# Kernel optimization log

Hardware: AMD Instinct MI355X
Metric: run time of the kernel (lower is better)

## Reference

```python
import jax, jax.numpy as jnp
import numpy as np

N = 8192          # total nodes (bipartite: first half left, second half right)
E = 65536         # raw edges
D = 256           # emb_dim
H = 8             # heads
HD = D // H       # head_dim = 32
EAD = 2           # edge_attr_dim


def _init(k, shape, fan_in):
    return (jax.random.normal(k, shape, jnp.float32) / np.sqrt(fan_in)).astype(jnp.float32)


def setup_inputs() -> dict:
    key = jax.random.key(0)
    ks = jax.random.split(key, 16)
    x = jax.random.normal(ks[0], (N, D), jnp.float32)
    src = jax.random.randint(ks[1], (E,), 0, N // 2, jnp.int32)
    dst = jax.random.randint(ks[2], (E,), N // 2, N, jnp.int32)
    edge_index = jnp.stack([src, dst])                       # [2, E]
    edge_attr = jax.random.uniform(ks[3], (E, EAD), jnp.float32)
    query_mask = jax.random.randint(ks[4], (E,), 0, 2, jnp.int32).astype(bool)
    return {
        "x": x,
        "edge_index": edge_index,
        "edge_attr": edge_attr,
        "query_mask": query_mask,
        "start_right": N // 2,
        "W_kqv": _init(ks[5], (D, 3 * D), D), "b_kqv": jnp.zeros((3 * D,), jnp.float32),
        "W_edge": _init(ks[6], (EAD, D), EAD), "b_edge": jnp.zeros((D,), jnp.float32),
        "W_att1": _init(ks[7], (3 * HD, HD), 3 * HD), "b_att1": jnp.zeros((HD,), jnp.float32),
        "W_att2": _init(ks[8], (HD, 1), HD), "b_att2": jnp.zeros((1,), jnp.float32),
        "W_out": _init(ks[9], (D, D), D), "b_out": jnp.zeros((D,), jnp.float32),
        "bn_gamma": jnp.ones((D,), jnp.float32), "bn_beta": jnp.zeros((D,), jnp.float32),
    }


def _build_graph(edge_index, query_mask, n):
    """Replicates MetaGNN.forward edge preprocessing (static, int-only)."""
    ei = np.asarray(edge_index)
    qm = np.asarray(query_mask).astype(bool)
    sup = np.where(~qm)[0]                                   # support edges
    # cat([edge_index[:, support], edge_index.flip(0)], dim=1)
    src = np.concatenate([ei[0, sup], ei[1]])
    dst = np.concatenate([ei[1, sup], ei[0]])
    attr_idx = np.concatenate([sup, np.arange(ei.shape[1])])
    # remove_self_loops
    keep = src != dst
    src, dst, attr_idx = src[keep], dst[keep], attr_idx[keep]
    # add_self_loops with fill_value [0, 0]
    loops = np.arange(n)
    src = np.concatenate([src, loops])
    dst = np.concatenate([dst, loops])
    return jnp.asarray(src), jnp.asarray(dst), jnp.asarray(attr_idx)


def _layer(x, src, dst, ea, W_kqv, b_kqv, W_edge, b_edge, W_att1, b_att1,
           W_att2, b_att2, W_out, b_out, bn_gamma, bn_beta):
    n = x.shape[0]
    kqv = x @ W_kqv + b_kqv                                  # [N, 3D]
    q = kqv[dst, :D].reshape(-1, H, HD)                      # x_i (target)
    k = kqv[src, D:2 * D].reshape(-1, H, HD) / np.sqrt(HD)   # x_j (source)
    v = kqv[src, 2 * D:].reshape(-1, H, HD)
    ef = jax.nn.relu((ea @ W_edge + b_edge).reshape(-1, H, HD))
    feat = jnp.concatenate([k, q, ef], axis=-1)              # [E, H, 3*HD]
    hdn = jax.nn.relu(jnp.einsum('ehf,fd->ehd', feat, W_att1) + b_att1)
    logits = (jnp.einsum('ehd,do->eho', hdn, W_att2) + b_att2)[..., 0]  # [E, H]
    # scatter-softmax over destination node segments
    m = jax.ops.segment_max(logits, dst, num_segments=n)
    a = jnp.exp(logits - m[dst])
    s = jax.ops.segment_sum(a, dst, num_segments=n)
    alpha = a / (s[dst] + 1e-16)                             # [E, H]
    msg = (alpha[..., None] * v).reshape(-1, D) @ W_out + b_out
    out = jax.ops.segment_sum(msg, dst, num_segments=n) + x  # aggr='add' + residual
    # BatchNorm1d (training-mode batch statistics, eps=1e-5)
    mu = out.mean(axis=0)
    var = out.var(axis=0)
    return (out - mu) / jnp.sqrt(var + 1e-5) * bn_gamma + bn_beta


def reference(x, edge_index, edge_attr, query_mask, start_right,
              W_kqv, b_kqv, W_edge, b_edge, W_att1, b_att1, W_att2, b_att2,
              W_out, b_out, bn_gamma, bn_beta):
    n = x.shape[0]
    src, dst, attr_idx = _build_graph(edge_index, query_mask, n)
    ea = jnp.concatenate(
        [edge_attr[attr_idx], jnp.zeros((n, edge_attr.shape[1]), edge_attr.dtype)], axis=0)
    return _layer(x, src, dst, ea, W_kqv, b_kqv, W_edge, b_edge,
                  W_att1, b_att1, W_att2, b_att2, W_out, b_out, bn_gamma, bn_beta)
```

## Files before the change

kernel.cpp:

```cpp
#include <hip/hip_runtime.h>

#define N_NODES 8192
#define E_RAW   65536
#define NSLOT   (2*E_RAW + N_NODES)
#define DEGCAP  48
#define L_ITER  4
#define MAIN_BLKS (E_RAW / (16 * L_ITER))
#define TAIL_BLKS (N_NODES / (16 * L_ITER))

typedef __attribute__((ext_vector_type(8)))  short bf16x8;
typedef __attribute__((ext_vector_type(4)))  short bf16x4;
typedef __attribute__((ext_vector_type(4)))  float f32x4;
typedef __attribute__((ext_vector_type(16))) float f32x16;
typedef unsigned short u16;

__device__ __forceinline__ u16 f2b(float f) {
  unsigned u = __float_as_uint(f);
  u = (u + 0x7FFFu + ((u >> 16) & 1u)) >> 16;
  return (u16)u;
}
__device__ __forceinline__ float b2f(u16 b) {
  return __uint_as_float(((unsigned)b) << 16);
}

__global__ __launch_bounds__(256) void setup_k(
    const float* __restrict__ x, u16* __restrict__ xb,
    const float* __restrict__ W_kqv, const float* __restrict__ b_kqv,
    const float* __restrict__ W_att1, const float* __restrict__ b_att1,
    const float* __restrict__ W_edge, const float* __restrict__ b_edge,
    const float* __restrict__ W_out,
    u16* __restrict__ BcatT, float* __restrict__ biascat,
    u16* __restrict__ wa1t, u16* __restrict__ WoutT, float* __restrict__ beW,
    int4* __restrict__ zbase)
{
  __shared__ float tile[64][65];
  const float inv_sqrt_hd = 0.17677669529663687f;
  int bx = blockIdx.x, t = threadIdx.x;

  if (bx < 2048) {
    int i = bx * 256 + t;
    float4 v = ((const float4*)x)[i];
    ushort4 o;
    o.x = f2b(v.x); o.y = f2b(v.y); o.z = f2b(v.z); o.w = f2b(v.w);
    ((ushort4*)xb)[i] = o;
    return;
  }
  if (bx < 2836) {
    int c = bx - 2048;
    int i = t;
    if (c < 768) {
      float v;
      if (c < 256) {
        int h = c >> 5, d2 = c & 31;
        float s = 0.f;
        #pragma unroll
        for (int j = 0; j < 32; ++j)
          s += W_kqv[i*768 + 256 + h*32 + j] * W_att1[j*32 + d2];
        v = s * inv_sqrt_hd;
      } else if (c < 512) {
        int c2 = c - 256; int h = c2 >> 5, d2 = c2 & 31;
        float s = 0.f;
        #pragma unroll
        for (int j = 0; j < 32; ++j)
          s += W_kqv[i*768 + h*32 + j] * W_att1[(32+j)*32 + d2];
        v = s;
      } else {
        v = W_kqv[i*768 + c];
      }
      BcatT[(size_t)c * 256 + i] = f2b(v);
      if (i == 0) {
        float bv;
        if (c < 256) {
          int h = c >> 5, d2 = c & 31;
          float s = 0.f;
          for (int j = 0; j < 32; ++j)
            s += b_kqv[256 + h*32 + j] * W_att1[j*32 + d2];
          bv = s * inv_sqrt_hd;
        } else if (c < 512) {
          int c2 = c - 256; int h = c2 >> 5, d2 = c2 & 31;
          float s = 0.f;
          for (int j = 0; j < 32; ++j)
            s += b_kqv[h*32 + j] * W_att1[(32+j)*32 + d2];
          bv = s + b_att1[c2 & 31];
        } else {
          bv = b_kqv[c];
        }
        biascat[c] = bv;
      }
    } else if (c < 772) {
      int idx = (c - 768) * 256 + i;
      int d2 = idx >> 5, j = idx & 31;
      wa1t[idx] = f2b(W_att1[(64 + j) * 32 + d2]);
    } else {
      int b = c - 772;
      int r0 = (b >> 2) * 64, c0 = (b & 3) * 64;
      for (int idx = i; idx < 4096; idx += 256) {
        int r = idx >> 6, cc = idx & 63;
        tile[r][cc] = W_out[(size_t)(r0 + r) * 256 + c0 + cc];
      }
      __syncthreads();
      for (int idx = i; idx < 4096; idx += 256) {
        int cc = idx >> 6, r = idx & 63;
        WoutT[(size_t)(c0 + cc) * 256 + r0 + r] = f2b(tile[r][cc]);
      }
    }
    return;
  }
  if (bx == 2836) {
    int h = t >> 5, d2 = t & 31;
    float s = 0.f;
    #pragma unroll
    for (int f = 0; f < 32; ++f)
      s += fmaxf(b_edge[h*32 + f], 0.f) * W_att1[(64 + f)*32 + d2];
    beW[h*32 + d2] = s;
    return;
  }
  int i = (bx - 2837) * 256 + t;
  if (i < 2176) zbase[i] = make_int4(0, 0, 0, 0);
}

__global__ __launch_bounds__(256) void gemm_scatter_k(
    const u16* __restrict__ xb, const u16* __restrict__ BcatT,
    const float* __restrict__ biascat, u16* __restrict__ nodeF,
    const int* __restrict__ ei, const int* __restrict__ qm,
    int* __restrict__ cnt, int* __restrict__ csr)
{
  int bx = blockIdx.x, t = threadIdx.x;
  if (bx < 768) {
    int lane = t & 63, wid = t >> 6;
    int cb = bx % 12, rb = bx / 12;
    int r0 = rb * 128 + wid * 32;
    int c0 = cb * 64;
    int lr = lane & 15, lk = (lane >> 4) * 8;
    f32x4 acc0[4] = {}, acc1[4] = {};
    for (int k0 = 0; k0 < 256; k0 += 32) {
      bf16x8 a0 = *(const bf16x8*)&xb[(size_t)(r0 + lr) * 256 + k0 + lk];
      bf16x8 a1 = *(const bf16x8*)&xb[(size_t)(r0 + 16 + lr) * 256 + k0 + lk];
      bf16x8 b0 = *(const bf16x8*)&BcatT[(size_t)(c0 + lr) * 256 + k0 + lk];
      bf16x8 b1 = *(const bf16x8*)&BcatT[(size_t)(c0 + 16 + lr) * 256 + k0 + lk];
      bf16x8 b2 = *(const bf16x8*)&BcatT[(size_t)(c0 + 32 + lr) * 256 + k0 + lk];
      bf16x8 b3 = *(const bf16x8*)&BcatT[(size_t)(c0 + 48 + lr) * 256 + k0 + lk];
      acc0[0] = __builtin_amdgcn_mfma_f32_16x16x32_bf16(a0, b0, acc0[0], 0, 0, 0);
      acc0[1] = __builtin_amdgcn_mfma_f32_16x16x32_bf16(a0, b1, acc0[1], 0, 0, 0);
      acc0[2] = __builtin_amdgcn_mfma_f32_16x16x32_bf16(a0, b2, acc0[2], 0, 0, 0);
      acc0[3] = __builtin_amdgcn_mfma_f32_16x16x32_bf16(a0, b3, acc0[3], 0, 0, 0);
      acc1[0] = __builtin_amdgcn_mfma_f32_16x16x32_bf16(a1, b0, acc1[0], 0, 0, 0);
      acc1[1] = __builtin_amdgcn_mfma_f32_16x16x32_bf16(a1, b1, acc1[1], 0, 0, 0);
      acc1[2] = __builtin_amdgcn_mfma_f32_16x16x32_bf16(a1, b2, acc1[2], 0, 0, 0);
      acc1[3] = __builtin_amdgcn_mfma_f32_16x16x32_bf16(a1, b3, acc1[3], 0, 0, 0);
    }
    int rbase = r0 + (lane >> 4) * 4;
    #pragma unroll
    for (int cc = 0; cc < 4; ++cc) {
      float bias = biascat[c0 + cc*16 + lr];
      #pragma unroll
      for (int r = 0; r < 4; ++r) {
        nodeF[(size_t)(rbase + r) * 768 + c0 + cc*16 + lr]      = f2b(acc0[cc][r] + bias);
        nodeF[(size_t)(rbase + 16 + r) * 768 + c0 + cc*16 + lr] = f2b(acc1[cc][r] + bias);
      }
    }
    return;
  }
  int slot = (bx - 768) * 256 + t;
  if (slot >= NSLOT) return;
  int src, dst;
  if (slot < E_RAW) {
    if (qm[slot] != 0) return;
    src = ei[slot]; dst = ei[E_RAW + slot];
  } else if (slot < 2*E_RAW) {
    int e = slot - E_RAW;
    src = ei[E_RAW + e]; dst = ei[e];
  } else {
    int n = slot - 2*E_RAW;
    src = n; dst = n;
  }
  int pos = atomicAdd(&cnt[dst], 1);
  if (pos < DEGCAP) csr[dst*DEGCAP + pos] = (slot << 13) | src;
}

__global__ __launch_bounds__(256) void logits_k(
    const int* __restrict__ ei, const int* __restrict__ qm,
    const float* __restrict__ eattr, const u16* __restrict__ nf,
    const u16* __restrict__ wa1t,
    const float* __restrict__ W_edge, const float* __restrict__ b_edge,
    const float* __restrict__ W_att2, const float* __restrict__ beW,
    float* __restrict__ lgd)
{
  __shared__ __align__(16) u16 kqls[4][16][8][40];

  int bx = blockIdx.x, t = threadIdx.x, lane = t & 63, wid = t >> 6;
  int col = lane & 31;
  int e = col >> 3, h = col & 7, hi = lane >> 5;

  float w2r[16];
  #pragma unroll
  for (int r = 0; r < 16; ++r)
    w2r[r] = W_att2[(r & 3) + 8*(r >> 2) + 4*hi];

  if (bx < MAIN_BLKS) {
    float ce0[16], ce1[16], cbe[16];
    #pragma unroll
    for (int i = 0; i < 8; ++i) {
      int fA = hi*8 + i, fB = 16 + hi*8 + i;
      ce0[i]   = W_edge[h*32 + fA];       ce0[8+i] = W_edge[h*32 + fB];
      ce1[i]   = W_edge[256 + h*32 + fA]; ce1[8+i] = W_edge[256 + h*32 + fB];
      cbe[i]   = b_edge[h*32 + fA];       cbe[8+i] = b_edge[h*32 + fB];
    }
    bf16x8 af0 = *(const bf16x8*)&wa1t[(lane & 31)*32 + hi*8];
    bf16x8 af1 = *(const bf16x8*)&wa1t[(lane & 31)*32 + 16 + hi*8];

    int eqm_r[L_ITER]; float2 ea_r[L_ITER];
    #pragma unroll
    for (int it = 0; it < L_ITER; ++it) {
      int er = ((bx * L_ITER + it) * 4 + wid) * 4 + e;
      eqm_r[it] = qm[er];
      ea_r[it] = *(const float2*)&eattr[2*er];
    }

    int nidx[2][8];
    #pragma unroll
    for (int m = 0; m < 8; ++m) {
      int erow = ((bx * L_ITER + 0) * 4 + wid) * 4 + (m & 3);
      nidx[0][m] = (m >> 2) ? ei[E_RAW + erow] : ei[erow];
    }

    #pragma unroll
    for (int it = 0; it < L_ITER; ++it) {
      if (it + 1 < L_ITER) {
        #pragma unroll
        for (int m = 0; m < 8; ++m) {
          int erow = ((bx * L_ITER + it + 1) * 4 + wid) * 4 + (m & 3);
          nidx[(it+1) & 1][m] = (m >> 2) ? ei[E_RAW + erow] : ei[erow];
        }
      }
      #pragma unroll
      for (int m = 0; m < 8; ++m) {
        bf16x8 v = *(const bf16x8*)&nf[(size_t)nidx[it & 1][m]*768 + lane*8];
        int drow = ((lane >> 5) << 3) + ((m >> 2) << 2) + (m & 3);
        int chunk = lane & 31;
        *(bf16x8*)&kqls[wid][drow][chunk >> 2][(chunk & 3)*8] = v;
      }

      float2 ea = ea_r[it];
      bf16x8 bf0, bf1;
      #pragma unroll
      for (int i = 0; i < 8; ++i) {
        float v0 = fmaf(ea.x, ce0[i],   fmaf(ea.y, ce1[i],   cbe[i]));
        float v1 = fmaf(ea.x, ce0[8+i], fmaf(ea.y, ce1[8+i], cbe[8+i]));
        bf0[i] = (short)f2b(fmaxf(v0, 0.f));
        bf1[i] = (short)f2b(fmaxf(v1, 0.f));
      }
      f32x16 acc = {};
      acc = __builtin_amdgcn_mfma_f32_32x32x16_bf16(af0, bf0, acc, 0, 0, 0);
      acc = __builtin_amdgcn_mfma_f32_32x32x16_bf16(af1, bf1, acc, 0, 0, 0);

      __builtin_amdgcn_wave_barrier();

      float lg0 = 0.f, lg1 = 0.f;
      #pragma unroll
      for (int q = 0; q < 4; ++q) {
        int off = q*8 + 4*hi;
        bf16x4 k0 = *(const bf16x4*)&kqls[wid][e][h][off];
        bf16x4 q0 = *(const bf16x4*)&kqls[wid][12 + e][h][off];
        bf16x4 k1 = *(const bf16x4*)&kqls[wid][4 + e][h][off];
        bf16x4 q1 = *(const bf16x4*)&kqls[wid][8 + e][h][off];
        #pragma unroll
        for (int j = 0; j < 4; ++j) {
          int r = q*4 + j;
          float efw = acc[r];
          float p0 = efw + b2f((u16)k0[j]) + b2f((u16)q0[j]);
          float p1 = efw + b2f((u16)k1[j]) + b2f((u16)q1[j]);
          lg0 = fmaf(fmaxf(p0, 0.f), w2r[r], lg0);
          lg1 = fmaf(fmaxf(p1, 0.f), w2r[r], lg1);
        }
      }
      lg0 += __shfl_xor(lg0, 32);
      lg1 += __shfl_xor(lg1, 32);
      int er = ((bx * L_ITER + it) * 4 + wid) * 4 + e;
      if (hi == 0) {
        if (eqm_r[it] == 0) lgd[(size_t)er*8 + h] = lg0;
      } else {
        lgd[(size_t)(E_RAW + er)*8 + h] = lg1;
      }
      __builtin_amdgcn_wave_barrier();
    }
  } else {
    float bew[16];
    #pragma unroll
    for (int r = 0; r < 16; ++r)
      bew[r] = beW[h*32 + (r & 3) + 8*(r >> 2) + 4*hi];

    for (int it = 0; it < L_ITER; ++it) {
      int n0 = (((bx - MAIN_BLKS) * L_ITER + it) * 4 + wid) * 4;
      int nn = n0 + e;
      #pragma unroll
      for (int m = 0; m < 4; ++m) {
        bf16x8 v = *(const bf16x8*)&nf[(size_t)(n0 + m)*768 + lane*8];
        int drow = ((lane >> 5) << 2) + m;
        int chunk = lane & 31;
        *(bf16x8*)&kqls[wid][drow][chunk >> 2][(chunk & 3)*8] = v;
      }
      __builtin_amdgcn_wave_barrier();
      float lg0 = 0.f;
      #pragma unroll
      for (int q = 0; q < 4; ++q) {
        int off = q*8 + 4*hi;
        bf16x4 k0 = *(const bf16x4*)&kqls[wid][e][h][off];
        bf16x4 q0 = *(const bf16x4*)&kqls[wid][4 + e][h][off];
        #pragma unroll
        for (int j = 0; j < 4; ++j) {
          int r = q*4 + j;
          float p = bew[r] + b2f((u16)k0[j]) + b2f((u16)q0[j]);
          lg0 = fmaf(fmaxf(p, 0.f), w2r[r], lg0);
        }
      }
      lg0 += __shfl_xor(lg0, 32);
      if (hi == 0) lgd[(size_t)(2*E_RAW + nn)*8 + h] = lg0;
      __builtin_amdgcn_wave_barrier();
    }
  }
}

__global__ __launch_bounds__(256) void aggr_k(const int* __restrict__ cnt,
                                              const int* __restrict__ csr,
                                              const float* __restrict__ lgd,
                                              const u16* __restrict__ nf,
                                              u16* __restrict__ aggb) {
  int t = threadIdx.x, lane = t & 63, wid = t >> 6;
  int n = blockIdx.x * 4 + wid;
  int deg = cnt[n]; if (deg > DEGCAP) deg = DEGCAP;
  int head = lane >> 3;

  int pk = (lane < deg) ? csr[n*DEGCAP + lane] : 0;

  const u16* vb = nf + 512 + lane * 4;
  int pk0 = __shfl(pk, 0);
  float lg_pf = lgd[(size_t)((unsigned)pk0 >> 13)*8 + head];
  bf16x4 v_pf = *(const bf16x4*)&vb[(size_t)(pk0 & 8191) * 768];

  float m = -3.4e38f, s = 0.f;
  float ac0 = 0.f, ac1 = 0.f, ac2 = 0.f, ac3 = 0.f;
  for (int i = 0; i < deg; ++i) {
    float lgv = lg_pf;
    bf16x4 v = v_pf;
    if (i + 1 < deg) {
      int pkn = __shfl(pk, i + 1);
      lg_pf = lgd[(size_t)((unsigned)pkn >> 13)*8 + head];
      v_pf = *(const bf16x4*)&vb[(size_t)(pkn & 8191) * 768];
    }
    float mn = fmaxf(m, lgv);
    float r = __expf(m - mn);
    float a = __expf(lgv - mn);
    s  = fmaf(s, r, a);
    ac0 = fmaf(ac0, r, a * b2f((u16)v[0]));
    ac1 = fmaf(ac1, r, a * b2f((u16)v[1]));
    ac2 = fmaf(ac2, r, a * b2f((u16)v[2]));
    ac3 = fmaf(ac3, r, a * b2f((u16)v[3]));
    m = mn;
  }
  float sinv = 1.f / (s + 1e-16f);
  ushort4 o;
  o.x = f2b(ac0 * sinv); o.y = f2b(ac1 * sinv);
  o.z = f2b(ac2 * sinv); o.w = f2b(ac3 * sinv);
  *(ushort4*)&aggb[(size_t)n * 256 + lane * 4] = o;
}

__global__ __launch_bounds__(256) void gemmout_k(const u16* __restrict__ aggb,
                                                 const u16* __restrict__ WoutT,
                                                 const float* __restrict__ x,
                                                 const int* __restrict__ cnt,
                                                 const float* __restrict__ b_out,
                                                 float* __restrict__ out,
                                                 float* __restrict__ bnsum,
                                                 float* __restrict__ bnsq) {
  int t = threadIdx.x, lane = t & 63, wid = t >> 6;
  int bx = blockIdx.x;
  int cb = bx & 3, rb = bx >> 2;
  int r0 = rb * 128 + wid * 32;
  int c0 = cb * 64;
  int lr = lane & 15, lk = (lane >> 4) * 8;
  f32x4 acc0[4] = {}, acc1[4] = {};
  for (int k0 = 0; k0 < 256; k0 += 32) {
    bf16x8 a0 = *(const bf16x8*)&aggb[(size_t)(r0 + lr) * 256 + k0 + lk];
    bf16x8 a1 = *(const bf16x8*)&aggb[(size_t)(r0 + 16 + lr) * 256 + k0 + lk];
    bf16x8 b0 = *(const bf16x8*)&WoutT[(size_t)(c0 + lr) * 256 + k0 + lk];
    bf16x8 b1 = *(const bf16x8*)&WoutT[(size_t)(c0 + 16 + lr) * 256 + k0 + lk];
    bf16x8 b2 = *(const bf16x8*)&WoutT[(size_t)(c0 + 32 + lr) * 256 + k0 + lk];
    bf16x8 b3 = *(const bf16x8*)&WoutT[(size_t)(c0 + 48 + lr) * 256 + k0 + lk];
    acc0[0] = __builtin_amdgcn_mfma_f32_16x16x32_bf16(a0, b0, acc0[0], 0, 0, 0);
    acc0[1] = __builtin_amdgcn_mfma_f32_16x16x32_bf16(a0, b1, acc0[1], 0, 0, 0);
    acc0[2] = __builtin_amdgcn_mfma_f32_16x16x32_bf16(a0, b2, acc0[2], 0, 0, 0);
    acc0[3] = __builtin_amdgcn_mfma_f32_16x16x32_bf16(a0, b3, acc0[3], 0, 0, 0);
    acc1[0] = __builtin_amdgcn_mfma_f32_16x16x32_bf16(a1, b0, acc1[0], 0, 0, 0);
    acc1[1] = __builtin_amdgcn_mfma_f32_16x16x32_bf16(a1, b1, acc1[1], 0, 0, 0);
    acc1[2] = __builtin_amdgcn_mfma_f32_16x16x32_bf16(a1, b2, acc1[2], 0, 0, 0);
    acc1[3] = __builtin_amdgcn_mfma_f32_16x16x32_bf16(a1, b3, acc1[3], 0, 0, 0);
  }
  int rbase = r0 + (lane >> 4) * 4;
  float degA[4], degB[4];
  #pragma unroll
  for (int r = 0; r < 4; ++r) {
    degA[r] = (float)cnt[rbase + r];
    degB[r] = (float)cnt[rbase + 16 + r];
  }
  #pragma unroll
  for (int cc = 0; cc < 4; ++cc) {
    int colC = c0 + cc*16 + lr;
    float bC = b_out[colC];
    float sC = 0.f, qC = 0.f;
    #pragma unroll
    for (int r = 0; r < 4; ++r) {
      int rowA = rbase + r, rowB = rbase + 16 + r;
      float v0 = acc0[cc][r] + x[(size_t)rowA * 256 + colC] + degA[r] * bC;
      float v1 = acc1[cc][r] + x[(size_t)rowB * 256 + colC] + degB[r] * bC;
      out[(size_t)rowA * 256 + colC] = v0;
      out[(size_t)rowB * 256 + colC] = v1;
      sC += v0 + v1; qC += v0*v0 + v1*v1;
    }
    #pragma unroll
    for (int msk = 16; msk <= 32; msk <<= 1) {
      sC += __shfl_xor(sC, msk); qC += __shfl_xor(qC, msk);
    }
    if (lane < 16) {
      atomicAdd(&bnsum[colC], sC); atomicAdd(&bnsq[colC], qC);
    }
  }
}

__global__ __launch_bounds__(256) void bnapply_k(float* __restrict__ out,
                                                 const float* __restrict__ bnsum,
                                                 const float* __restrict__ bnsq,
                                                 const float* __restrict__ gamma,
                                                 const float* __restrict__ beta) {
  int t = threadIdx.x;
  int c4 = t & 63;
  int r = blockIdx.x * 4 + (t >> 6);
  float4 s4 = ((const float4*)bnsum)[c4];
  float4 q4 = ((const float4*)bnsq)[c4];
  float4 g4 = ((const float4*)gamma)[c4];
  float4 b4 = ((const float4*)beta)[c4];
  float4 v = ((const float4*)out)[(size_t)r * 64 + c4];
  #pragma unroll
  for (int j = 0; j < 4; ++j) {
    float mu = (&s4.x)[j] * (1.f / 8192.f);
    float var = (&q4.x)[j] * (1.f / 8192.f) - mu*mu;
    float inv = rsqrtf(var + 1e-5f);
    (&v.x)[j] = ((&v.x)[j] - mu) * inv * (&g4.x)[j] + (&b4.x)[j];
  }
  ((float4*)out)[(size_t)r * 64 + c4] = v;
}

extern "C" void kernel_launch(void* const* d_in, const int* in_sizes, int n_in,
                              void* d_out, int out_size, void* d_ws, size_t ws_size,
                              hipStream_t stream) {
  (void)in_sizes; (void)n_in; (void)out_size; (void)ws_size;
  const float* x      = (const float*)d_in[0];
  const int*   ei     = (const int*)d_in[1];
  const float* eattr  = (const float*)d_in[2];
  const int*   qm     = (const int*)d_in[3];
  const float* W_kqv  = (const float*)d_in[5];
  const float* b_kqv  = (const float*)d_in[6];
  const float* W_edge = (const float*)d_in[7];
  const float* b_edge = (const float*)d_in[8];
  const float* W_att1 = (const float*)d_in[9];
  const float* b_att1 = (const float*)d_in[10];
  const float* W_att2 = (const float*)d_in[11];
  const float* W_out  = (const float*)d_in[13];
  const float* b_out  = (const float*)d_in[14];
  const float* gamma  = (const float*)d_in[15];
  const float* beta   = (const float*)d_in[16];
  float* out = (float*)d_out;

  char* w = (char*)d_ws;
  u16*    xb      = (u16*)w;     w += (size_t)N_NODES*256*2;
  u16*    BcatT   = (u16*)w;     w += (size_t)768*256*2;
  u16*    wa1t    = (u16*)w;     w += 1024*2;
  u16*    WoutT   = (u16*)w;     w += (size_t)256*256*2;
  u16*    nodeFb  = (u16*)w;     w += (size_t)N_NODES*768*2;
  float*  biascat = (float*)w;   w += 768*4;
  float*  beW     = (float*)w;   w += 256*4;
  u16*    aggb    = (u16*)w;     w += (size_t)N_NODES*256*2;
  int*    cnt     = (int*)w;     w += N_NODES*4;
  float*  bnsum   = (float*)w;   w += 256*4;
  float*  bnsq    = (float*)w;   w += 256*4;
  int*    csr     = (int*)w;     w += (size_t)N_NODES*DEGCAP*4;
  float*  lgd     = (float*)w;   w += (size_t)NSLOT*8*4;

  setup_k<<<2846, 256, 0, stream>>>(
      x, xb, W_kqv, b_kqv, W_att1, b_att1, W_edge, b_edge, W_out,
      BcatT, biascat, wa1t, WoutT, beW, (int4*)cnt);

  gemm_scatter_k<<<768 + (NSLOT + 255)/256, 256, 0, stream>>>(
      xb, BcatT, biascat, nodeFb, ei, qm, cnt, csr);

  logits_k<<<MAIN_BLKS + TAIL_BLKS, 256, 0, stream>>>(
      ei, qm, eattr, nodeFb, wa1t, W_edge, b_edge, W_att2, beW, lgd);

  aggr_k<<<N_NODES/4, 256, 0, stream>>>(cnt, csr, lgd, nodeFb, aggb);

  gemmout_k<<<256, 256, 0, stream>>>(
      aggb, WoutT, x, cnt, b_out, out, bnsum, bnsq);

  bnapply_k<<<N_NODES/4, 256, 0, stream>>>(out, bnsum, bnsq, gamma, beta);
}
```

Before: 98.00 us.

## Gather K/Q rows directly into LDS with global_load_lds and XOR swizzle

Replaces register-staged gathers of node K/Q features (global load, then LDS store) in the logits kernel with direct global-to-LDS loads into a flat, XOR-swizzled buffer, and reads them back through a swizzle-aware helper. The goal is to remove the VGPR round trip and LDS write instructions and to avoid bank conflicts on the readback. It also drops the software prefetch of edge indices one iteration ahead and adds explicit waitcnt and sched barriers, which serialise the index loads with the gather and may expose more latency.

Result: no change. 96.32 us (-1.7%).

```diff
diff --git a/kernel.cpp b/kernel.cpp
--- a/kernel.cpp
+++ b/kernel.cpp
@@ -21,6 +21,11 @@
 }
 __device__ __forceinline__ float b2f(u16 b) {
   return __uint_as_float(((unsigned)b) << 16);
+}
+
+__device__ __forceinline__ bf16x4 kq_rd(const char* wbase, int p, int h, int off) {
+  int byte = (p*512 + h*64 + off*2) ^ ((p & 7) << 4);
+  return *(const bf16x4*)(wbase + byte);
 }
 
 __global__ __launch_bounds__(256) void setup_k(
@@ -186,11 +191,12 @@
     const float* __restrict__ W_att2, const float* __restrict__ beW,
     float* __restrict__ lgd)
 {
-  __shared__ __align__(16) u16 kqls[4][16][8][40];
+  __shared__ __align__(16) char kq_raw[4][16*512];
 
   int bx = blockIdx.x, t = threadIdx.x, lane = t & 63, wid = t >> 6;
   int col = lane & 31;
   int e = col >> 3, h = col & 7, hi = lane >> 5;
+  char* wbase = kq_raw[wid];
 
   float w2r[16];
   #pragma unroll
@@ -217,28 +223,21 @@
       ea_r[it] = *(const float2*)&eattr[2*er];
     }
 
-    int nidx[2][8];
-    #pragma unroll
-    for (int m = 0; m < 8; ++m) {
-      int erow = ((bx * L_ITER + 0) * 4 + wid) * 4 + (m & 3);
-      nidx[0][m] = (m >> 2) ? ei[E_RAW + erow] : ei[erow];
-    }
-
     #pragma unroll
     for (int it = 0; it < L_ITER; ++it) {
-      if (it + 1 < L_ITER) {
-        #pragma unroll
-        for (int m = 0; m < 8; ++m) {
-          int erow = ((bx * L_ITER + it + 1) * 4 + wid) * 4 + (m & 3);
-          nidx[(it+1) & 1][m] = (m >> 2) ? ei[E_RAW + erow] : ei[erow];
-        }
-      }
+      asm volatile("s_waitcnt lgkmcnt(0)" ::: "memory");
+      __builtin_amdgcn_sched_barrier(0);
       #pragma unroll
       for (int m = 0; m < 8; ++m) {
-        bf16x8 v = *(const bf16x8*)&nf[(size_t)nidx[it & 1][m]*768 + lane*8];
-        int drow = ((lane >> 5) << 3) + ((m >> 2) << 2) + (m & 3);
-        int chunk = lane & 31;
-        *(bf16x8*)&kqls[wid][drow][chunk >> 2][(chunk & 3)*8] = v;
+        int erow = ((bx * L_ITER + it) * 4 + wid) * 4 + (m & 3);
+        int node = (m >> 2) ? ei[E_RAW + erow] : ei[erow];
+        int lo = ((m >> 2) << 2) + (m & 3);
+        int p = 2*lo + hi;
+        unsigned goff = (unsigned)((lane & 31) * 16) ^ (unsigned)((p & 7) << 4);
+        const char* src = (const char*)nf + (size_t)node*1536 + (size_t)hi*512 + goff;
+        __builtin_amdgcn_global_load_lds(
+            (const __attribute__((address_space(1))) void*)src,
+            (__attribute__((address_space(3))) void*)(wbase + lo*1024), 16, 0, 0);
       }
 
       float2 ea = ea_r[it];
@@ -254,16 +253,18 @@
       acc = __builtin_amdgcn_mfma_f32_32x32x16_bf16(af0, bf0, acc, 0, 0, 0);
       acc = __builtin_amdgcn_mfma_f32_32x32x16_bf16(af1, bf1, acc, 0, 0, 0);
 
+      asm volatile("s_waitcnt vmcnt(0)" ::: "memory");
+      __builtin_amdgcn_sched_barrier(0);
       __builtin_amdgcn_wave_barrier();
 
       float lg0 = 0.f, lg1 = 0.f;
       #pragma unroll
       for (int q = 0; q < 4; ++q) {
         int off = q*8 + 4*hi;
-        bf16x4 k0 = *(const bf16x4*)&kqls[wid][e][h][off];
-        bf16x4 q0 = *(const bf16x4*)&kqls[wid][12 + e][h][off];
-        bf16x4 k1 = *(const bf16x4*)&kqls[wid][4 + e][h][off];
-        bf16x4 q1 = *(const bf16x4*)&kqls[wid][8 + e][h][off];
+        bf16x4 k0 = kq_rd(wbase, 2*e,     h, off);
+        bf16x4 q0 = kq_rd(wbase, 2*e + 9, h, off);
+        bf16x4 k1 = kq_rd(wbase, 2*e + 8, h, off);
+        bf16x4 q1 = kq_rd(wbase, 2*e + 1, h, off);
         #pragma unroll
         for (int j = 0; j < 4; ++j) {
           int r = q*4 + j;
@@ -293,20 +294,27 @@
     for (int it = 0; it < L_ITER; ++it) {
       int n0 = (((bx - MAIN_BLKS) * L_ITER + it) * 4 + wid) * 4;
       int nn = n0 + e;
+      asm volatile("s_waitcnt lgkmcnt(0)" ::: "memory");
+      __builtin_amdgcn_sched_barrier(0);
       #pragma unroll
       for (int m = 0; m < 4; ++m) {
-        bf16x8 v = *(const bf16x8*)&nf[(size_t)(n0 + m)*768 + lane*8];
-        int drow = ((lane >> 5) << 2) + m;
-        int chunk = lane & 31;
-        *(bf16x8*)&kqls[wid][drow][chunk >> 2][(chunk & 3)*8] = v;
-      }
+        int node = n0 + m;
+        int p = 2*m + hi;
+        unsigned goff = (unsigned)((lane & 31) * 16) ^ (unsigned)((p & 7) << 4);
+        const char* src = (const char*)nf + (size_t)node*1536 + (size_t)hi*512 + goff;
+        __builtin_amdgcn_global_load_lds(
+            (const __attribute__((address_space(1))) void*)src,
+            (__attribute__((address_space(3))) void*)(wbase + m*1024), 16, 0, 0);
+      }
+      asm volatile("s_waitcnt vmcnt(0)" ::: "memory");
+      __builtin_amdgcn_sched_barrier(0);
       __builtin_amdgcn_wave_barrier();
       float lg0 = 0.f;
       #pragma unroll
       for (int q = 0; q < 4; ++q) {
         int off = q*8 + 4*hi;
-        bf16x4 k0 = *(const bf16x4*)&kqls[wid][e][h][off];
-        bf16x4 q0 = *(const bf16x4*)&kqls[wid][4 + e][h][off];
+        bf16x4 k0 = kq_rd(wbase, 2*e,     h, off);
+        bf16x4 q0 = kq_rd(wbase, 2*e + 1, h, off);
         #pragma unroll
         for (int j = 0; j < 4; ++j) {
           int r = q*4 + j;
```
